# Kernel tuning notes

Measured on AMD Instinct MI355X. Metric: run time of the kernel, lower is better.

The kernel has to match this reference:

```python
import jax, jax.numpy as jnp
import numpy as np

# Block-sparse causal local attention (DeepSpeed SparseSelfAttention math):
#   scores = SDD(Q, K^T) on nonzero layout blocks
#   scores = masked_fill(block-causal mask == 0, -inf)
#   probs  = sparse_softmax(scores * head_dim**-0.5)  (rpe=None, key_padding_mask=None)
#   out    = DSD(probs, V)
# Layout: block (i, j) is nonzero iff 0 <= i - j < W (causal sliding window of W blocks).

BSZ, H, S, D = 2, 8, 4096, 64
BLK = 32          # sparsity block size
W = 16            # number of local key blocks per query block (512-token window)


def setup_inputs() -> dict:
    key = jax.random.key(0)
    kq, kk, kv = jax.random.split(key, 3)
    query = jax.random.normal(kq, (BSZ, H, S, D), jnp.float32)
    k = jax.random.normal(kk, (BSZ, H, S, D), jnp.float32)
    v = jax.random.normal(kv, (BSZ, H, S, D), jnp.float32)
    return {"query": query, "key": k, "value": v}


def reference(query, key, value):
    b, h, s, d = query.shape
    nb = s // BLK
    scaling = float(d) ** -0.5

    qb = query.reshape(b, h, nb, BLK, d)
    kb = key.reshape(b, h, nb, BLK, d)
    vb = value.reshape(b, h, nb, BLK, d)

    blk_i = jnp.arange(nb)
    # key-block indices attended by each query block: i-W+1 ... i   [nb, W]
    k_idx = blk_i[:, None] + jnp.arange(-(W - 1), 1)[None, :]
    blk_valid = k_idx >= 0
    k_idx_c = jnp.maximum(k_idx, 0)

    Kg = kb[:, :, k_idx_c]   # [b, h, nb, W, BLK, d]
    Vg = vb[:, :, k_idx_c]   # [b, h, nb, W, BLK, d]

    # block-sparse SDD: only the W local blocks per query block are computed
    scores = jnp.einsum('bhnqd,bhnwkd->bhnqwk', qb, Kg) * scaling

    # token-level causal mask (covers the diagonal-block triangular mask
    # from make_sparse_attn_mask) + validity of gathered blocks
    qpos = blk_i[:, None] * BLK + jnp.arange(BLK)[None, :]           # [nb, BLK]
    kpos = k_idx_c[..., None] * BLK + jnp.arange(BLK)                # [nb, W, BLK]
    allowed = blk_valid[:, None, :, None] & (kpos[:, None, :, :] <= qpos[:, :, None, None])
    scores = jnp.where(allowed[None, None], scores, -jnp.inf)

    # fused sparse softmax over all present key positions of each query row
    probs = jax.nn.softmax(scores.reshape(b, h, nb, BLK, W * BLK), axis=-1)
    probs = probs.reshape(b, h, nb, BLK, W, BLK)

    # block-sparse DSD
    out = jnp.einsum('bhnqwk,bhnwkd->bhnqd', probs, Vg)
    return out.reshape(b, h, s, d)
```

## Files before the change

kernel.cpp:

```cpp
#include <hip/hip_runtime.h>
#include <hip/hip_bf16.h>


#define NH    8
#define SEQ   4096
#define DIM   64
#define NBLK  128
#define WIN   16
#define QG    4
#define GROUPS (NBLK / QG)

typedef __bf16 bf16x8 __attribute__((ext_vector_type(8)));
typedef __bf16 bf16x4 __attribute__((ext_vector_type(4)));
typedef float  f32x4  __attribute__((ext_vector_type(4)));
typedef unsigned short u16;
typedef unsigned int   u32;

#define KSTR 72
#define VSTR 40
#define DTHR 8.0f

__device__ __forceinline__ bf16x8 cvt8(f32x4 a, f32x4 b) {
    bf16x8 r;
#pragma unroll
    for (int j = 0; j < 4; ++j) { r[j] = (__bf16)a[j]; r[4 + j] = (__bf16)b[j]; }
    return r;
}

__global__ __launch_bounds__(256)
void sparse_attn_v14(const float* __restrict__ Q,
                     const float* __restrict__ K,
                     const float* __restrict__ V,
                     float* __restrict__ O)
{
    const int b  = (int)blockIdx.x;
    const int lg = (b & 7) * 64 + (b >> 3);
    const int bh = lg >> 5;
    const int n0 = (lg & 31) * QG;

    const int t    = (int)threadIdx.x;
    const int wave = t >> 6;
    const int lane = t & 63;
    const int l15  = lane & 15;
    const int l4   = lane >> 4;
    const int nq   = n0 + wave;

    __shared__ u16 Kt[2][32][KSTR];
    __shared__ u16 Vt[2][64][VSTR];

    const size_t base = (size_t)bh * SEQ * DIM;
    const float SC = 0.125f * 1.44269504088896340736f;

    const int skrow = t >> 3;
    const int skc   = (t & 7) * 8;
    const int svkey = (t & 15) * 2;
    const int svdg  = t >> 4;

    bf16x8 qf[2][2];
#pragma unroll
    for (int rt = 0; rt < 2; ++rt) {
        const float* qp = Q + base + (size_t)(nq * 32 + rt * 16 + l15) * DIM + l4 * 8;
        f32x4 a0 = *(const f32x4*)qp        * SC;
        f32x4 b0 = *(const f32x4*)(qp + 4)  * SC;
        f32x4 a1 = *(const f32x4*)(qp + 32) * SC;
        f32x4 b1 = *(const f32x4*)(qp + 36) * SC;
        qf[rt][0] = cvt8(a0, b0);
        qf[rt][1] = cvt8(a1, b1);
    }

    f32x4 acc[2][4] = {};
    float m[2]  = {-1e30f, -1e30f};
    float lp[2] = {0.f, 0.f};

    const int kb0 = (n0 >= WIN - 1) ? n0 - (WIN - 1) : 0;
    const int kb1 = n0 + QG - 1;

    f32x4 kra, krb, vra, vrb;
    {
        const float* kp = K + base + (size_t)(kb0 * 32 + skrow) * DIM + skc;
        kra = *(const f32x4*)kp;  krb = *(const f32x4*)(kp + 4);
        const float* vp = V + base + (size_t)(kb0 * 32 + svkey) * DIM + svdg * 4;
        vra = *(const f32x4*)vp;  vrb = *(const f32x4*)(vp + DIM);
    }
    {
        *(bf16x8*)&Kt[0][skrow][skc] = cvt8(kra, krb);
#pragma unroll
        for (int j = 0; j < 4; ++j) {
            u32 w = (u32)__builtin_bit_cast(u16, (__bf16)vra[j])
                  | ((u32)__builtin_bit_cast(u16, (__bf16)vrb[j]) << 16);
            *(u32*)&Vt[0][svdg * 4 + j][svkey] = w;
        }
    }
    __syncthreads();

    int cur = 0;
    for (int kb = kb0; kb <= kb1; ++kb) {
        const bool haveNext = (kb < kb1);

        if (haveNext) {
            const float* kp = K + base + (size_t)((kb + 1) * 32 + skrow) * DIM + skc;
            kra = *(const f32x4*)kp;  krb = *(const f32x4*)(kp + 4);
            const float* vp = V + base + (size_t)((kb + 1) * 32 + svkey) * DIM + svdg * 4;
            vra = *(const f32x4*)vp;  vrb = *(const f32x4*)(vp + DIM);
        }

        const bool part = (kb <= nq) && (kb >= nq - (WIN - 1));
        if (part) {
            bf16x8 kf[2][2];
#pragma unroll
            for (int kh = 0; kh < 2; ++kh)
#pragma unroll
                for (int c = 0; c < 2; ++c)
                    kf[kh][c] = *(const bf16x8*)&Kt[cur][kh * 16 + l15][c * 32 + l4 * 8];

            bf16x8 vf[4];
#pragma unroll
            for (int dt = 0; dt < 4; ++dt) {
                bf16x4 lo = *(const bf16x4*)&Vt[cur][dt * 16 + l15][l4 * 4];
                bf16x4 hi = *(const bf16x4*)&Vt[cur][dt * 16 + l15][16 + l4 * 4];
#pragma unroll
                for (int j = 0; j < 4; ++j) { vf[dt][j] = lo[j]; vf[dt][4 + j] = hi[j]; }
            }

            f32x4 s[2][2];
#pragma unroll
            for (int rt = 0; rt < 2; ++rt)
#pragma unroll
                for (int kh = 0; kh < 2; ++kh) {
                    f32x4 a = {};
                    a = __builtin_amdgcn_mfma_f32_16x16x32_bf16(kf[kh][0], qf[rt][0], a, 0, 0, 0);
                    a = __builtin_amdgcn_mfma_f32_16x16x32_bf16(kf[kh][1], qf[rt][1], a, 0, 0, 0);
                    s[rt][kh] = a;
                }

            if (kb == nq) {
#pragma unroll
                for (int rt = 0; rt < 2; ++rt)
#pragma unroll
                    for (int kh = 0; kh < 2; ++kh)
#pragma unroll
                        for (int r = 0; r < 4; ++r)
                            if (kh * 16 + l4 * 4 + r > rt * 16 + l15)
                                s[rt][kh][r] = -1e30f;
            }

            bool ok = true;
#pragma unroll
            for (int rt = 0; rt < 2; ++rt)
#pragma unroll
                for (int kh = 0; kh < 2; ++kh)
#pragma unroll
                    for (int r = 0; r < 4; ++r)
                        ok &= (s[rt][kh][r] <= m[rt] + DTHR);

            if (!__all(ok)) {
#pragma unroll
                for (int rt = 0; rt < 2; ++rt) {
                    float t0 = -1e30f;
#pragma unroll
                    for (int kh = 0; kh < 2; ++kh)
#pragma unroll
                        for (int r = 0; r < 4; ++r) t0 = fmaxf(t0, s[rt][kh][r]);
                    t0 = fmaxf(t0, __shfl_xor(t0, 16));
                    t0 = fmaxf(t0, __shfl_xor(t0, 32));
                    const float mn = fmaxf(m[rt], t0);
                    const float al = exp2f(m[rt] - mn);
                    m[rt] = mn;
                    lp[rt] *= al;
#pragma unroll
                    for (int dt = 0; dt < 4; ++dt)
#pragma unroll
                        for (int r = 0; r < 4; ++r) acc[rt][dt][r] *= al;
                }
            }

            bf16x8 pbf[2];
#pragma unroll
            for (int rt = 0; rt < 2; ++rt) {
                float psum = 0.f;
#pragma unroll
                for (int j = 0; j < 8; ++j) {
                    const float p = exp2f(s[rt][j >> 2][j & 3] - m[rt]);
                    psum += p;
                    pbf[rt][j] = (__bf16)p;
                }
                lp[rt] += psum;
            }

#pragma unroll
            for (int rt = 0; rt < 2; ++rt)
#pragma unroll
                for (int dt = 0; dt < 4; ++dt)
                    acc[rt][dt] = __builtin_amdgcn_mfma_f32_16x16x32_bf16(
                        vf[dt], pbf[rt], acc[rt][dt], 0, 0, 0);
        }

        if (haveNext) {
            *(bf16x8*)&Kt[cur ^ 1][skrow][skc] = cvt8(kra, krb);
#pragma unroll
            for (int j = 0; j < 4; ++j) {
                u32 w = (u32)__builtin_bit_cast(u16, (__bf16)vra[j])
                      | ((u32)__builtin_bit_cast(u16, (__bf16)vrb[j]) << 16);
                *(u32*)&Vt[cur ^ 1][svdg * 4 + j][svkey] = w;
            }
        }

        __syncthreads();
        cur ^= 1;
    }

#pragma unroll
    for (int rt = 0; rt < 2; ++rt) {
        float ps = lp[rt];
        ps += __shfl_xor(ps, 16);
        ps += __shfl_xor(ps, 32);
        const float inv = 1.0f / ps;
        float* op = O + base + (size_t)(nq * 32 + rt * 16 + l15) * DIM + l4 * 4;
#pragma unroll
        for (int dt = 0; dt < 4; ++dt) {
            f32x4 v;
#pragma unroll
            for (int r = 0; r < 4; ++r) v[r] = acc[rt][dt][r] * inv;
            *(f32x4*)(op + dt * 16) = v;
        }
    }
}

extern "C" void kernel_launch(void* const* d_in, const int* in_sizes, int n_in,
                              void* d_out, int out_size, void* d_ws, size_t ws_size,
                              hipStream_t stream)
{
    const float* Q = (const float*)d_in[0];
    const float* K = (const float*)d_in[1];
    const float* V = (const float*)d_in[2];
    float*       O = (float*)d_out;

    const int nwg = 2 * NH * GROUPS;
    hipLaunchKernelGGL(sparse_attn_v14, dim3(nwg), dim3(256), 0, stream,
                       Q, K, V, O);
}
```

Baseline: 36.99 us.

## Split each query block's key window across two waves and merge via LDS

```diff
diff --git a/kernel.cpp b/kernel.cpp
--- a/kernel.cpp
+++ b/kernel.cpp
@@ -7,7 +7,7 @@
 #define DIM   64
 #define NBLK  128
 #define WIN   16
-#define QG    4
+#define QG    2
 #define GROUPS (NBLK / QG)
 
 typedef __bf16 bf16x8 __attribute__((ext_vector_type(8)));
@@ -28,25 +28,30 @@
 }
 
 __global__ __launch_bounds__(256)
-void sparse_attn_v14(const float* __restrict__ Q,
+void sparse_attn_v16(const float* __restrict__ Q,
                      const float* __restrict__ K,
                      const float* __restrict__ V,
                      float* __restrict__ O)
 {
     const int b  = (int)blockIdx.x;
-    const int lg = (b & 7) * 64 + (b >> 3);
-    const int bh = lg >> 5;
-    const int n0 = (lg & 31) * QG;
+    const int lg = (b & 7) * 128 + (b >> 3);
+    const int bh = lg >> 6;
+    const int n0 = (lg & 63) * QG;
 
     const int t    = (int)threadIdx.x;
     const int wave = t >> 6;
     const int lane = t & 63;
     const int l15  = lane & 15;
     const int l4   = lane >> 4;
-    const int nq   = n0 + wave;
-
-    __shared__ u16 Kt[2][32][KSTR];
-    __shared__ u16 Vt[2][64][VSTR];
+    const int qi   = wave >> 1;
+    const int half = wave & 1;
+    const int nq   = n0 + qi;
+
+    __shared__ __align__(16) char smem[19712];
+    u16 (*Kt)[32][KSTR]   = (u16 (*)[32][KSTR])smem;
+    u16 (*Vt)[64][VSTR]   = (u16 (*)[64][VSTR])(smem + 9216);
+    float (*accsh)[32][64] = (float (*)[32][64])smem;
+    float (*mlsh)[4][64]   = (float (*)[4][64])(smem + 16384);
 
     const size_t base = (size_t)bh * SEQ * DIM;
     const float SC = 0.125f * 1.44269504088896340736f;
@@ -72,6 +77,10 @@
     float m[2]  = {-1e30f, -1e30f};
     float lp[2] = {0.f, 0.f};
 
+    const int kbs = (nq >= WIN - 1) ? nq - (WIN - 1) : 0;
+    const int lo  = half ? ((nq - 7 > kbs) ? nq - 7 : kbs) : kbs;
+    const int hi  = half ? nq : nq - 8;
+
     const int kb0 = (n0 >= WIN - 1) ? n0 - (WIN - 1) : 0;
     const int kb1 = n0 + QG - 1;
 
@@ -104,8 +113,7 @@
             vra = *(const f32x4*)vp;  vrb = *(const f32x4*)(vp + DIM);
         }
 
-        const bool part = (kb <= nq) && (kb >= nq - (WIN - 1));
-        if (part) {
+        if (kb >= lo && kb <= hi) {
             bf16x8 kf[2][2];
 #pragma unroll
             for (int kh = 0; kh < 2; ++kh)
@@ -116,10 +124,10 @@
             bf16x8 vf[4];
 #pragma unroll
             for (int dt = 0; dt < 4; ++dt) {
-                bf16x4 lo = *(const bf16x4*)&Vt[cur][dt * 16 + l15][l4 * 4];
-                bf16x4 hi = *(const bf16x4*)&Vt[cur][dt * 16 + l15][16 + l4 * 4];
-#pragma unroll
-                for (int j = 0; j < 4; ++j) { vf[dt][j] = lo[j]; vf[dt][4 + j] = hi[j]; }
+                bf16x4 vlo = *(const bf16x4*)&Vt[cur][dt * 16 + l15][l4 * 4];
+                bf16x4 vhi = *(const bf16x4*)&Vt[cur][dt * 16 + l15][16 + l4 * 4];
+#pragma unroll
+                for (int j = 0; j < 4; ++j) { vf[dt][j] = vlo[j]; vf[dt][4 + j] = vhi[j]; }
             }
 
             f32x4 s[2][2];
@@ -180,9 +188,9 @@
                 float psum = 0.f;
 #pragma unroll
                 for (int j = 0; j < 8; ++j) {
-                    const float p = exp2f(s[rt][j >> 2][j & 3] - m[rt]);
-                    psum += p;
-                    pbf[rt][j] = (__bf16)p;
+                    const float pv = exp2f(s[rt][j >> 2][j & 3] - m[rt]);
+                    psum += pv;
+                    pbf[rt][j] = (__bf16)pv;
                 }
                 lp[rt] += psum;
             }
@@ -209,19 +217,49 @@
         cur ^= 1;
     }
 
+    float l[2];
 #pragma unroll
     for (int rt = 0; rt < 2; ++rt) {
         float ps = lp[rt];
         ps += __shfl_xor(ps, 16);
         ps += __shfl_xor(ps, 32);
-        const float inv = 1.0f / ps;
-        float* op = O + base + (size_t)(nq * 32 + rt * 16 + l15) * DIM + l4 * 4;
-#pragma unroll
-        for (int dt = 0; dt < 4; ++dt) {
-            f32x4 v;
-#pragma unroll
-            for (int r = 0; r < 4; ++r) v[r] = acc[rt][dt][r] * inv;
-            *(f32x4*)(op + dt * 16) = v;
+        l[rt] = ps;
+    }
+
+    if (half == 1) {
+#pragma unroll
+        for (int rt = 0; rt < 2; ++rt) {
+            mlsh[qi][rt][lane]     = m[rt];
+            mlsh[qi][2 + rt][lane] = l[rt];
+#pragma unroll
+            for (int dt = 0; dt < 4; ++dt)
+#pragma unroll
+                for (int r = 0; r < 4; ++r)
+                    accsh[qi][rt * 16 + dt * 4 + r][lane] = acc[rt][dt][r];
+        }
+    }
+
+    __syncthreads();
+
+    if (half == 0) {
+#pragma unroll
+        for (int rt = 0; rt < 2; ++rt) {
+            const float m2 = mlsh[qi][rt][lane];
+            const float l2 = mlsh[qi][2 + rt][lane];
+            const float mn = fmaxf(m[rt], m2);
+            const float a1 = exp2f(m[rt] - mn);
+            const float a2 = exp2f(m2 - mn);
+            const float inv = 1.0f / (l[rt] * a1 + l2 * a2);
+            float* op = O + base + (size_t)(nq * 32 + rt * 16 + l15) * DIM + l4 * 4;
+#pragma unroll
+            for (int dt = 0; dt < 4; ++dt) {
+                f32x4 v;
+#pragma unroll
+                for (int r = 0; r < 4; ++r)
+                    v[r] = (acc[rt][dt][r] * a1 +
+                            accsh[qi][rt * 16 + dt * 4 + r][lane] * a2) * inv;
+                *(f32x4*)(op + dt * 16) = v;
+            }
         }
     }
 }
@@ -236,6 +274,6 @@
     float*       O = (float*)d_out;
 
     const int nwg = 2 * NH * GROUPS;
-    hipLaunchKernelGGL(sparse_attn_v14, dim3(nwg), dim3(256), 0, stream,
+    hipLaunchKernelGGL(sparse_attn_v16, dim3(nwg), dim3(256), 0, stream,
                        Q, K, V, O);
 }
```

Result: slower. 53.53 us (+44.7%).

## Split each query block across two waves and halve query blocks per workgroup

Applied to the files above, without the earlier changes.

```diff
diff --git a/kernel.cpp b/kernel.cpp
--- a/kernel.cpp
+++ b/kernel.cpp
@@ -7,7 +7,7 @@
 #define DIM   64
 #define NBLK  128
 #define WIN   16
-#define QG    4
+#define QG    2
 #define GROUPS (NBLK / QG)
 
 typedef __bf16 bf16x8 __attribute__((ext_vector_type(8)));
@@ -28,22 +28,24 @@
 }
 
 __global__ __launch_bounds__(256)
-void sparse_attn_v14(const float* __restrict__ Q,
+void sparse_attn_v18(const float* __restrict__ Q,
                      const float* __restrict__ K,
                      const float* __restrict__ V,
                      float* __restrict__ O)
 {
     const int b  = (int)blockIdx.x;
-    const int lg = (b & 7) * 64 + (b >> 3);
-    const int bh = lg >> 5;
-    const int n0 = (lg & 31) * QG;
+    const int lg = (b & 7) * 128 + (b >> 3);
+    const int bh = lg >> 6;
+    const int n0 = (lg & 63) * QG;
 
     const int t    = (int)threadIdx.x;
     const int wave = t >> 6;
     const int lane = t & 63;
     const int l15  = lane & 15;
     const int l4   = lane >> 4;
-    const int nq   = n0 + wave;
+    const int qi   = wave >> 1;
+    const int rh   = wave & 1;
+    const int nq   = n0 + qi;
 
     __shared__ u16 Kt[2][32][KSTR];
     __shared__ u16 Vt[2][64][VSTR];
@@ -56,22 +58,22 @@
     const int svkey = (t & 15) * 2;
     const int svdg  = t >> 4;
 
-    bf16x8 qf[2][2];
-#pragma unroll
-    for (int rt = 0; rt < 2; ++rt) {
-        const float* qp = Q + base + (size_t)(nq * 32 + rt * 16 + l15) * DIM + l4 * 8;
+    bf16x8 qf[2];
+    {
+        const float* qp = Q + base + (size_t)(nq * 32 + rh * 16 + l15) * DIM + l4 * 8;
         f32x4 a0 = *(const f32x4*)qp        * SC;
         f32x4 b0 = *(const f32x4*)(qp + 4)  * SC;
         f32x4 a1 = *(const f32x4*)(qp + 32) * SC;
         f32x4 b1 = *(const f32x4*)(qp + 36) * SC;
-        qf[rt][0] = cvt8(a0, b0);
-        qf[rt][1] = cvt8(a1, b1);
-    }
-
-    f32x4 acc[2][4] = {};
-    float m[2]  = {-1e30f, -1e30f};
-    float lp[2] = {0.f, 0.f};
-
+        qf[0] = cvt8(a0, b0);
+        qf[1] = cvt8(a1, b1);
+    }
+
+    f32x4 acc[4] = {};
+    float m  = -1e30f;
+    float lp = 0.f;
+
+    const int lo  = (nq >= WIN - 1) ? nq - (WIN - 1) : 0;
     const int kb0 = (n0 >= WIN - 1) ? n0 - (WIN - 1) : 0;
     const int kb1 = n0 + QG - 1;
 
@@ -104,8 +106,7 @@
             vra = *(const f32x4*)vp;  vrb = *(const f32x4*)(vp + DIM);
         }
 
-        const bool part = (kb <= nq) && (kb >= nq - (WIN - 1));
-        if (part) {
+        if (kb >= lo && kb <= nq) {
             bf16x8 kf[2][2];
 #pragma unroll
             for (int kh = 0; kh < 2; ++kh)
@@ -116,83 +117,69 @@
             bf16x8 vf[4];
 #pragma unroll
             for (int dt = 0; dt < 4; ++dt) {
-                bf16x4 lo = *(const bf16x4*)&Vt[cur][dt * 16 + l15][l4 * 4];
-                bf16x4 hi = *(const bf16x4*)&Vt[cur][dt * 16 + l15][16 + l4 * 4];
-#pragma unroll
-                for (int j = 0; j < 4; ++j) { vf[dt][j] = lo[j]; vf[dt][4 + j] = hi[j]; }
-            }
-
-            f32x4 s[2][2];
-#pragma unroll
-            for (int rt = 0; rt < 2; ++rt)
-#pragma unroll
-                for (int kh = 0; kh < 2; ++kh) {
-                    f32x4 a = {};
-                    a = __builtin_amdgcn_mfma_f32_16x16x32_bf16(kf[kh][0], qf[rt][0], a, 0, 0, 0);
-                    a = __builtin_amdgcn_mfma_f32_16x16x32_bf16(kf[kh][1], qf[rt][1], a, 0, 0, 0);
-                    s[rt][kh] = a;
-                }
+                bf16x4 vlo = *(const bf16x4*)&Vt[cur][dt * 16 + l15][l4 * 4];
+                bf16x4 vhi = *(const bf16x4*)&Vt[cur][dt * 16 + l15][16 + l4 * 4];
+#pragma unroll
+                for (int j = 0; j < 4; ++j) { vf[dt][j] = vlo[j]; vf[dt][4 + j] = vhi[j]; }
+            }
+
+            f32x4 s[2];
+#pragma unroll
+            for (int kh = 0; kh < 2; ++kh) {
+                f32x4 a = {};
+                a = __builtin_amdgcn_mfma_f32_16x16x32_bf16(kf[kh][0], qf[0], a, 0, 0, 0);
+                a = __builtin_amdgcn_mfma_f32_16x16x32_bf16(kf[kh][1], qf[1], a, 0, 0, 0);
+                s[kh] = a;
+            }
 
             if (kb == nq) {
 #pragma unroll
-                for (int rt = 0; rt < 2; ++rt)
-#pragma unroll
-                    for (int kh = 0; kh < 2; ++kh)
-#pragma unroll
-                        for (int r = 0; r < 4; ++r)
-                            if (kh * 16 + l4 * 4 + r > rt * 16 + l15)
-                                s[rt][kh][r] = -1e30f;
+                for (int kh = 0; kh < 2; ++kh)
+#pragma unroll
+                    for (int r = 0; r < 4; ++r)
+                        if (kh * 16 + l4 * 4 + r > rh * 16 + l15)
+                            s[kh][r] = -1e30f;
             }
 
             bool ok = true;
 #pragma unroll
-            for (int rt = 0; rt < 2; ++rt)
+            for (int kh = 0; kh < 2; ++kh)
+#pragma unroll
+                for (int r = 0; r < 4; ++r)
+                    ok &= (s[kh][r] <= m + DTHR);
+
+            if (!__all(ok)) {
+                float t0 = -1e30f;
 #pragma unroll
                 for (int kh = 0; kh < 2; ++kh)
 #pragma unroll
-                    for (int r = 0; r < 4; ++r)
-                        ok &= (s[rt][kh][r] <= m[rt] + DTHR);
-
-            if (!__all(ok)) {
-#pragma unroll
-                for (int rt = 0; rt < 2; ++rt) {
-                    float t0 = -1e30f;
-#pragma unroll
-                    for (int kh = 0; kh < 2; ++kh)
-#pragma unroll
-                        for (int r = 0; r < 4; ++r) t0 = fmaxf(t0, s[rt][kh][r]);
-                    t0 = fmaxf(t0, __shfl_xor(t0, 16));
-                    t0 = fmaxf(t0, __shfl_xor(t0, 32));
-                    const float mn = fmaxf(m[rt], t0);
-                    const float al = exp2f(m[rt] - mn);
-                    m[rt] = mn;
-                    lp[rt] *= al;
-#pragma unroll
-                    for (int dt = 0; dt < 4; ++dt)
-#pragma unroll
-                        for (int r = 0; r < 4; ++r) acc[rt][dt][r] *= al;
-                }
-            }
-
-            bf16x8 pbf[2];
-#pragma unroll
-            for (int rt = 0; rt < 2; ++rt) {
-                float psum = 0.f;
-#pragma unroll
-                for (int j = 0; j < 8; ++j) {
-                    const float p = exp2f(s[rt][j >> 2][j & 3] - m[rt]);
-                    psum += p;
-                    pbf[rt][j] = (__bf16)p;
-                }
-                lp[rt] += psum;
-            }
-
-#pragma unroll
-            for (int rt = 0; rt < 2; ++rt)
+                    for (int r = 0; r < 4; ++r) t0 = fmaxf(t0, s[kh][r]);
+                t0 = fmaxf(t0, __shfl_xor(t0, 16));
+                t0 = fmaxf(t0, __shfl_xor(t0, 32));
+                const float mn = fmaxf(m, t0);
+                const float al = exp2f(m - mn);
+                m = mn;
+                lp *= al;
 #pragma unroll
                 for (int dt = 0; dt < 4; ++dt)
-                    acc[rt][dt] = __builtin_amdgcn_mfma_f32_16x16x32_bf16(
-                        vf[dt], pbf[rt], acc[rt][dt], 0, 0, 0);
+#pragma unroll
+                    for (int r = 0; r < 4; ++r) acc[dt][r] *= al;
+            }
+
+            bf16x8 pbf;
+            float psum = 0.f;
+#pragma unroll
+            for (int j = 0; j < 8; ++j) {
+                const float pv = exp2f(s[j >> 2][j & 3] - m);
+                psum += pv;
+                pbf[j] = (__bf16)pv;
+            }
+            lp += psum;
+
+#pragma unroll
+            for (int dt = 0; dt < 4; ++dt)
+                acc[dt] = __builtin_amdgcn_mfma_f32_16x16x32_bf16(
+                    vf[dt], pbf, acc[dt], 0, 0, 0);
         }
 
         if (haveNext) {
@@ -209,18 +196,17 @@
         cur ^= 1;
     }
 
-#pragma unroll
-    for (int rt = 0; rt < 2; ++rt) {
-        float ps = lp[rt];
+    {
+        float ps = lp;
         ps += __shfl_xor(ps, 16);
         ps += __shfl_xor(ps, 32);
         const float inv = 1.0f / ps;
-        float* op = O + base + (size_t)(nq * 32 + rt * 16 + l15) * DIM + l4 * 4;
+        float* op = O + base + (size_t)(nq * 32 + rh * 16 + l15) * DIM + l4 * 4;
 #pragma unroll
         for (int dt = 0; dt < 4; ++dt) {
             f32x4 v;
 #pragma unroll
-            for (int r = 0; r < 4; ++r) v[r] = acc[rt][dt][r] * inv;
+            for (int r = 0; r < 4; ++r) v[r] = acc[dt][r] * inv;
             *(f32x4*)(op + dt * 16) = v;
         }
     }
@@ -236,6 +222,6 @@
     float*       O = (float*)d_out;
 
     const int nwg = 2 * NH * GROUPS;
-    hipLaunchKernelGGL(sparse_attn_v14, dim3(nwg), dim3(256), 0, stream,
+    hipLaunchKernelGGL(sparse_attn_v18, dim3(nwg), dim3(256), 0, stream,
                        Q, K, V, O);
 }
```

New measurement: 37.12 us. About the same (+0.3%).
